# Kernel optimization log

Measured on AMD Instinct MI355X. Metric: run time of the kernel, lower is better.

The kernel has to match this reference:

```python
import jax, jax.numpy as jnp
import numpy as np

OSC_TIME = 10
UNITS = 256
D_IN = 256
BATCH = 32
SEQLEN = 2000


def setup_inputs() -> dict:
    key = jax.random.key(0)
    k1, k2, k3 = jax.random.split(key, 3)
    scale = 1.0 / np.sqrt(UNITS)
    x = jax.random.normal(k1, (BATCH, SEQLEN, D_IN), dtype=jnp.float32)
    W_x = jax.random.normal(k2, (4, 2, D_IN, UNITS), dtype=jnp.float32) * scale
    W_h = jax.random.normal(k3, (4, 2, UNITS, UNITS), dtype=jnp.float32) * scale
    b_x = jnp.zeros((4, 2, UNITS), dtype=jnp.float32)
    b_h = jnp.zeros((4, 2, UNITS), dtype=jnp.float32)
    return {"x": x, "W_x": W_x, "b_x": b_x, "W_h": W_h, "b_h": b_h}


def reference(x, W_x, b_x, W_h, b_h):
    # Subsample every OSC_TIME steps (tf.gather stride)
    xs = x[:, ::OSC_TIME]                       # [B, Ts, D]
    B, Ts, _ = xs.shape
    U = W_h.shape[-1]

    # Precompute input projections for all 4 cells x 2 gates: [4,2,B,Ts,U]
    xp = jnp.einsum('btd,cgdu->cgbtu', xs, W_x) + b_x[:, :, None, None, :]

    h0 = jnp.zeros((4, B, U), dtype=x.dtype)

    def ff_step(h, xp_t):                       # h [4,B,U], xp_t [4,2,B,U]
        hp = jnp.einsum('cbu,cguv->cgbv', h, W_h) + b_h[:, :, None, :]
        g = jax.nn.sigmoid(xp_t + hp)           # [4,2,B,U]
        j, k = g[:, 0], g[:, 1]
        h_new = j * (1.0 - h) + (1.0 - k) * h   # flip-flop update
        return h_new, h_new

    _, hs = jax.lax.scan(ff_step, h0, jnp.moveaxis(xp, 3, 0))  # hs [Ts,4,B,U]
    phi, omega, r, mu = hs[:, 0], hs[:, 1], hs[:, 2], hs[:, 3]  # each [Ts,B,U]

    # Oscillator: emit z = r*cos(phi) then update r, phi; OSC_TIME sub-steps
    def osc_step(carry, _):
        r_t, phi_t = carry
        z = r_t * jnp.cos(phi_t)
        r_n = r_t + (mu - jnp.square(r_t)) * r_t
        phi_n = phi_t + omega
        return (r_n, phi_n), z

    _, zs = jax.lax.scan(osc_step, (r, phi), None, length=OSC_TIME)  # [S,Ts,B,U]
    out = jnp.transpose(zs, (2, 1, 0, 3)).reshape(B, Ts * OSC_TIME, U)
    return out
```

## Files before the change

### kernel.cpp

```cpp
#include <hip/hip_runtime.h>
#include <hip/hip_fp16.h>
#include <stdint.h>

#define TS 200

typedef _Float16 h2_t  __attribute__((ext_vector_type(2)));
typedef _Float16 f16x8 __attribute__((ext_vector_type(8)));
typedef float    f32x4 __attribute__((ext_vector_type(4)));

static __device__ __forceinline__ float fdot2f(uint32_t w, uint32_t h, float acc) {
#if __has_builtin(__builtin_amdgcn_fdot2)
    return __builtin_amdgcn_fdot2(__builtin_bit_cast(h2_t, w),
                                  __builtin_bit_cast(h2_t, h), acc, false);
#else
    h2_t a = __builtin_bit_cast(h2_t, w), b = __builtin_bit_cast(h2_t, h);
    acc = fmaf((float)a.x, (float)b.x, acc);
    acc = fmaf((float)a.y, (float)b.y, acc);
    return acc;
#endif
}

template <int CTRL>
static __device__ __forceinline__ float dpp_add(float x) {
    int m = __builtin_amdgcn_update_dpp(0, __builtin_bit_cast(int, x), CTRL, 0xF, 0xF, true);
    return x + __builtin_bit_cast(float, m);
}

__global__ __launch_bounds__(256) void pack_all(const float* __restrict__ x,
                                                const float* __restrict__ Wx,
                                                const float* __restrict__ Wh,
                                                _Float16* __restrict__ xh,
                                                _Float16* __restrict__ wxt,
                                                uint32_t* __restrict__ wp) {
    int bid = blockIdx.x, tid = threadIdx.x;
    if (bid < 6400) {
        int row = bid, col = tid;
        int b = row / 200, t = row - b * 200;
        xh[(size_t)row * 256 + col] = (_Float16)x[((size_t)(b * 2000 + t * 10)) * 256 + col];
    } else if (bid < 8448) {
        int n = bid - 6400, k = tid;
        wxt[(size_t)n * 256 + k] = (_Float16)Wx[((size_t)((n >> 8) * 256 + k)) * 256 + (n & 255)];
    } else {
        int idx = (bid - 8448) * 256 + tid;
        int e = idx & 3, thr = (idx >> 2) & 511, j = (idx >> 11) & 15;
        int g = (idx >> 15) & 1, c = idx >> 16;
        int vs = thr & 7, uq = (thr >> 3) & 7, wu = thr >> 6;
        int uu = j >> 2, i = j & 3;
        int u = wu * 32 + uq * 4 + uu;
        int v = vs * 32 + i * 8 + e * 2;
        const float* base = Wh + ((size_t)((c * 2 + g) * 256 + v)) * 256 + u;
        h2_t p; p.x = (_Float16)base[0]; p.y = (_Float16)base[256];
        wp[idx] = __builtin_bit_cast(uint32_t, p);
    }
}

__global__ __launch_bounds__(256) void xp_gemm(const _Float16* __restrict__ xh,
                                               const _Float16* __restrict__ wxt,
                                               const float* __restrict__ bxf,
                                               _Float16* __restrict__ xp) {
    __shared__ _Float16 As[128 * 64];
    __shared__ _Float16 Bs[128 * 64];
    const int tid = threadIdx.x;
    const int lane = tid & 63, w = tid >> 6;
    const int m0 = (blockIdx.x >> 4) * 128;
    const int n0 = (blockIdx.x & 15) * 128;
    const int mw = (w & 1) * 64, nw = (w >> 1) * 64;

    f32x4 acc[4][4] = {};

    for (int kb = 0; kb < 4; kb++) {
        const int k0 = kb * 64;
#pragma unroll
        for (int q = 0; q < 4; q++) {
            int ii = w * 4 + q;
            int r = ii * 8 + (lane >> 3);
            int kcol = (lane & 7) * 8;
            const _Float16* ga = xh  + (size_t)(m0 + r) * 256 + k0 + kcol;
            const _Float16* gb = wxt + (size_t)(n0 + r) * 256 + k0 + kcol;
            __builtin_amdgcn_global_load_lds(
                (const __attribute__((address_space(1))) uint32_t*)ga,
                (__attribute__((address_space(3))) uint32_t*)(As + ii * 512), 16, 0, 0);
            __builtin_amdgcn_global_load_lds(
                (const __attribute__((address_space(1))) uint32_t*)gb,
                (__attribute__((address_space(3))) uint32_t*)(Bs + ii * 512), 16, 0, 0);
        }
        __syncthreads();
#pragma unroll
        for (int kc = 0; kc < 2; kc++) {
            f16x8 a[4], b[4];
#pragma unroll
            for (int mt = 0; mt < 4; mt++)
                a[mt] = *(const f16x8*)&As[(mw + mt * 16 + (lane & 15)) * 64 + kc * 32 + (lane >> 4) * 8];
#pragma unroll
            for (int nt = 0; nt < 4; nt++)
                b[nt] = *(const f16x8*)&Bs[(nw + nt * 16 + (lane & 15)) * 64 + kc * 32 + (lane >> 4) * 8];
#pragma unroll
            for (int mt = 0; mt < 4; mt++)
#pragma unroll
                for (int nt = 0; nt < 4; nt++)
                    acc[mt][nt] = __builtin_amdgcn_mfma_f32_16x16x32_f16(a[mt], b[nt], acc[mt][nt], 0, 0, 0);
        }
        __syncthreads();
    }

    const int nl = lane & 15, quad = lane >> 4;
#pragma unroll
    for (int nt = 0; nt < 4; nt++) {
        int n = n0 + nw + nt * 16 + nl;
        float bias = bxf[n];
        int c = n >> 9, gu = n & 511;
#pragma unroll
        for (int mt = 0; mt < 4; mt++)
#pragma unroll
            for (int r = 0; r < 4; r++) {
                int m = m0 + mw + mt * 16 + quad * 4 + r;
                int b = m / 200, t = m - b * 200;
                xp[((size_t)((c * 32 + b) * 200 + t)) * 512 + gu] =
                    (_Float16)(acc[mt][nt][r] + bias);
            }
    }
}

__global__ __launch_bounds__(1024, 4) void recurrence(const _Float16* __restrict__ xp,
                                                      const float* __restrict__ bh,
                                                      const uint32_t* __restrict__ Wp,
                                                      float* __restrict__ hs) {
    const int c = blockIdx.x >> 5;
    const int b = blockIdx.x & 31;
    const int tid = threadIdx.x;
    const int g = tid >> 9;
    const int thr = tid & 511;
    const int lane = tid & 63;
    const int vs = lane & 7;
    const int uq = lane >> 3;
    const int wu = (tid >> 6) & 7;

    __shared__ __align__(16) uint32_t h2s[8 * 20];
    __shared__ float sg[512];

    uint4 w[16];
    {
        const uint4* wb = (const uint4*)Wp + ((size_t)(c * 2 + g) * 16) * 512 + thr;
#pragma unroll
        for (int j = 0; j < 16; j++) w[j] = wb[(size_t)j * 512];
    }
#pragma unroll
    for (int j = 0; j < 16; j++)
        asm volatile("" : "+v"(w[j].x), "+v"(w[j].y), "+v"(w[j].z), "+v"(w[j].w));

    const int u_w = wu * 32 + uq * 4 + vs;
    float bias = 0.f;
    const _Float16* xpb = nullptr;
    if (vs < 4) {
        bias = bh[(c * 2 + g) * 256 + u_w];
        xpb = xp + ((size_t)((c * 32 + b) * 200)) * 512 + g * 256 + u_w;
    }

    float hreg = 0.f;
    if (tid < 160) h2s[tid] = 0u;
    __syncthreads();

    const size_t hsb = (size_t)((c * 32 + b) * 200) * 256 + tid;

    for (int t = 0; t < TS; t++) {
        float xpv = 0.f;
        if (vs < 4) xpv = (float)xpb[(size_t)t * 512];

        uint4 hh[4];
#pragma unroll
        for (int i = 0; i < 4; i++) hh[i] = *(const uint4*)(h2s + vs * 20 + i * 4);

        float acc[4] = {0.f, 0.f, 0.f, 0.f};
#pragma unroll
        for (int uu = 0; uu < 4; uu++)
#pragma unroll
            for (int i = 0; i < 4; i++) {
                acc[uu] = fdot2f(w[uu * 4 + i].x, hh[i].x, acc[uu]);
                acc[uu] = fdot2f(w[uu * 4 + i].y, hh[i].y, acc[uu]);
                acc[uu] = fdot2f(w[uu * 4 + i].z, hh[i].z, acc[uu]);
                acc[uu] = fdot2f(w[uu * 4 + i].w, hh[i].w, acc[uu]);
            }
#pragma unroll
        for (int uu = 0; uu < 4; uu++) {
            float a = acc[uu];
            a = dpp_add<0xB1>(a);
            a = dpp_add<0x4E>(a);
            a = dpp_add<0x141>(a);
            acc[uu] = a;
        }
        if (vs < 4) {
            float s = (vs == 0 ? acc[0] : vs == 1 ? acc[1] : vs == 2 ? acc[2] : acc[3])
                      + xpv + bias;
            sg[u_w * 2 + g] = 1.f / (1.f + __expf(-s));
        }
        __syncthreads();
        if (tid < 256) {
            float2 jk = *(const float2*)(sg + tid * 2);
            float hn = jk.x + hreg * (1.f - jk.x - jk.y);
            hreg = hn;
            hs[hsb + (size_t)t * 256] = hn;
            ((_Float16*)h2s)[(tid >> 5) * 40 + (tid & 31)] = (_Float16)hn;
        }
        __syncthreads();
    }
}

__global__ __launch_bounds__(256) void osc(const float* __restrict__ hs,
                                           float* __restrict__ out) {
    int tid = blockIdx.x * 256 + threadIdx.x;
    const int cstride = 32 * 200 * 256;
    int u = tid & 255;
    int bt = tid >> 8;
    int t = bt % 200, b = bt / 200;
    float phi   = hs[0 * cstride + tid];
    float omega = hs[1 * cstride + tid];
    float r     = hs[2 * cstride + tid];
    float mu    = hs[3 * cstride + tid];
    float* o = out + ((size_t)(b * 2000 + t * 10)) * 256 + u;
#pragma unroll
    for (int s = 0; s < 10; s++) {
        o[(size_t)s * 256] = r * __cosf(phi);
        r = r + (mu - r * r) * r;
        phi = phi + omega;
    }
}

extern "C" void kernel_launch(void* const* d_in, const int* in_sizes, int n_in,
                              void* d_out, int out_size, void* d_ws, size_t ws_size,
                              hipStream_t stream) {
    const float* x  = (const float*)d_in[0];
    const float* Wx = (const float*)d_in[1];
    const float* bx = (const float*)d_in[2];
    const float* Wh = (const float*)d_in[3];
    const float* bh = (const float*)d_in[4];
    float* out = (float*)d_out;

    char* ws = (char*)d_ws;
    const size_t XP = (size_t)4 * 32 * 200 * 512 * 2;
    const size_t HS = (size_t)4 * 32 * 200 * 256 * 4;
    const size_t XH = (size_t)6400 * 256 * 2;

    _Float16* xp  = (_Float16*)ws;
    float*    hs  = (float*)(ws + XP);
    _Float16* xh  = (_Float16*)(ws + XP);
    _Float16* wxt = (_Float16*)(ws + XP + XH);
    uint32_t* wp  = (uint32_t*)(ws + XP + HS);

    pack_all<<<9472, 256, 0, stream>>>(x, Wx, Wh, xh, wxt, wp);
    xp_gemm<<<800, 256, 0, stream>>>(xh, wxt, bx, xp);
    recurrence<<<128, 1024, 0, stream>>>(xp, bh, wp, hs);
    osc<<<6400, 256, 0, stream>>>(hs, out);
}
```

Baseline: 390.1 us.

## Fuse both gates per wave and double-buffer hidden state to halve barriers

The recurrence work mapping changes so that each wave computes both j and k gates for a pair of units. The flip-flop update is then done in registers via DPP lane moves instead of through shared memory. The hidden-state buffer is double-buffered, which removes one of the two __syncthreads per timestep and the sg shared array. The Wh packing layout is changed to match. The cost is more cross-lane DPP shuffles, and the sigmoid is now computed in every lane rather than only in lanes with vs<4.

```diff
diff --git a/kernel.cpp b/kernel.cpp
--- a/kernel.cpp
+++ b/kernel.cpp
@@ -24,6 +24,11 @@
 static __device__ __forceinline__ float dpp_add(float x) {
     int m = __builtin_amdgcn_update_dpp(0, __builtin_bit_cast(int, x), CTRL, 0xF, 0xF, true);
     return x + __builtin_bit_cast(float, m);
+}
+template <int CTRL>
+static __device__ __forceinline__ float dpp_mov(float x) {
+    int m = __builtin_amdgcn_update_dpp(0, __builtin_bit_cast(int, x), CTRL, 0xF, 0xF, true);
+    return __builtin_bit_cast(float, m);
 }
 
 __global__ __launch_bounds__(256) void pack_all(const float* __restrict__ x,
@@ -42,11 +47,14 @@
         wxt[(size_t)n * 256 + k] = (_Float16)Wx[((size_t)((n >> 8) * 256 + k)) * 256 + (n & 255)];
     } else {
         int idx = (bid - 8448) * 256 + tid;
-        int e = idx & 3, thr = (idx >> 2) & 511, j = (idx >> 11) & 15;
-        int g = (idx >> 15) & 1, c = idx >> 16;
-        int vs = thr & 7, uq = (thr >> 3) & 7, wu = thr >> 6;
-        int uu = j >> 2, i = j & 3;
-        int u = wu * 32 + uq * 4 + uu;
+        int e   = idx & 3;
+        int thr = (idx >> 2) & 1023;
+        int j   = (idx >> 12) & 15;
+        int c   = idx >> 16;
+        int a = j >> 2, i = j & 3;
+        int uu = a >> 1, g = a & 1;
+        int vs = thr & 7, uq = (thr >> 3) & 7, wv = thr >> 6;
+        int u = (wv * 8 + uq) * 2 + uu;
         int v = vs * 32 + i * 8 + e * 2;
         const float* base = Wh + ((size_t)((c * 2 + g) * 256 + v)) * 256 + u;
         h2_t p; p.x = (_Float16)base[0]; p.y = (_Float16)base[256];
@@ -121,85 +129,90 @@
     }
 }
 
-__global__ __launch_bounds__(1024, 4) void recurrence(const _Float16* __restrict__ xp,
-                                                      const float* __restrict__ bh,
-                                                      const uint32_t* __restrict__ Wp,
-                                                      float* __restrict__ hs) {
-    const int c = blockIdx.x >> 5;
-    const int b = blockIdx.x & 31;
+__global__ __attribute__((amdgpu_flat_work_group_size(1024, 1024),
+                          amdgpu_waves_per_eu(4, 4)))
+void recurrence(const _Float16* __restrict__ xp,
+                const float* __restrict__ bh,
+                const uint32_t* __restrict__ Wp,
+                float* __restrict__ hs) {
+    const int cb  = blockIdx.x;
+    const int c   = cb >> 5;
     const int tid = threadIdx.x;
-    const int g = tid >> 9;
-    const int thr = tid & 511;
     const int lane = tid & 63;
     const int vs = lane & 7;
     const int uq = lane >> 3;
-    const int wu = (tid >> 6) & 7;
-
-    __shared__ __align__(16) uint32_t h2s[8 * 20];
-    __shared__ float sg[512];
+    const int wv = tid >> 6;
+    const int upair = wv * 8 + uq;
+    const int u0 = upair * 2;
+
+    __shared__ __align__(16) uint32_t h2s[2][160];
 
     uint4 w[16];
     {
-        const uint4* wb = (const uint4*)Wp + ((size_t)(c * 2 + g) * 16) * 512 + thr;
-#pragma unroll
-        for (int j = 0; j < 16; j++) w[j] = wb[(size_t)j * 512];
+        const uint4* wb = (const uint4*)Wp + (size_t)c * 16 * 1024 + tid;
+#pragma unroll
+        for (int j = 0; j < 16; j++) w[j] = wb[(size_t)j * 1024];
     }
 #pragma unroll
     for (int j = 0; j < 16; j++)
         asm volatile("" : "+v"(w[j].x), "+v"(w[j].y), "+v"(w[j].z), "+v"(w[j].w));
 
-    const int u_w = wu * 32 + uq * 4 + vs;
     float bias = 0.f;
     const _Float16* xpb = nullptr;
     if (vs < 4) {
-        bias = bh[(c * 2 + g) * 256 + u_w];
-        xpb = xp + ((size_t)((c * 32 + b) * 200)) * 512 + g * 256 + u_w;
+        int g_sel = vs & 1, u_sel = u0 + (vs >> 1);
+        bias = bh[(c * 2 + g_sel) * 256 + u_sel];
+        xpb  = xp + (size_t)cb * 200 * 512 + g_sel * 256 + u_sel;
     }
 
     float hreg = 0.f;
-    if (tid < 160) h2s[tid] = 0u;
+    if (tid < 160) { h2s[0][tid] = 0u; }
     __syncthreads();
 
-    const size_t hsb = (size_t)((c * 32 + b) * 200) * 256 + tid;
+    float* hsb = hs + (size_t)cb * 200 * 256 + u0;
+
+    const uint32_t* wf = (const uint32_t*)w;
 
     for (int t = 0; t < TS; t++) {
+        const uint32_t* hbuf = h2s[t & 1];
+        uint32_t* hnext = h2s[(t + 1) & 1];
+
         float xpv = 0.f;
         if (vs < 4) xpv = (float)xpb[(size_t)t * 512];
 
         uint4 hh[4];
 #pragma unroll
-        for (int i = 0; i < 4; i++) hh[i] = *(const uint4*)(h2s + vs * 20 + i * 4);
+        for (int i = 0; i < 4; i++) hh[i] = *(const uint4*)(hbuf + vs * 20 + i * 4);
+        const uint32_t* hf = (const uint32_t*)hh;
 
         float acc[4] = {0.f, 0.f, 0.f, 0.f};
 #pragma unroll
-        for (int uu = 0; uu < 4; uu++)
-#pragma unroll
-            for (int i = 0; i < 4; i++) {
-                acc[uu] = fdot2f(w[uu * 4 + i].x, hh[i].x, acc[uu]);
-                acc[uu] = fdot2f(w[uu * 4 + i].y, hh[i].y, acc[uu]);
-                acc[uu] = fdot2f(w[uu * 4 + i].z, hh[i].z, acc[uu]);
-                acc[uu] = fdot2f(w[uu * 4 + i].w, hh[i].w, acc[uu]);
-            }
-#pragma unroll
-        for (int uu = 0; uu < 4; uu++) {
-            float a = acc[uu];
-            a = dpp_add<0xB1>(a);
-            a = dpp_add<0x4E>(a);
-            a = dpp_add<0x141>(a);
-            acc[uu] = a;
-        }
-        if (vs < 4) {
-            float s = (vs == 0 ? acc[0] : vs == 1 ? acc[1] : vs == 2 ? acc[2] : acc[3])
-                      + xpv + bias;
-            sg[u_w * 2 + g] = 1.f / (1.f + __expf(-s));
-        }
-        __syncthreads();
-        if (tid < 256) {
-            float2 jk = *(const float2*)(sg + tid * 2);
-            float hn = jk.x + hreg * (1.f - jk.x - jk.y);
-            hreg = hn;
-            hs[hsb + (size_t)t * 256] = hn;
-            ((_Float16*)h2s)[(tid >> 5) * 40 + (tid & 31)] = (_Float16)hn;
+        for (int i = 0; i < 4; i++)
+#pragma unroll
+            for (int cmp = 0; cmp < 4; cmp++)
+#pragma unroll
+                for (int a = 0; a < 4; a++)
+                    acc[a] = fdot2f(wf[(a * 4 + i) * 4 + cmp], hf[i * 4 + cmp], acc[a]);
+
+#pragma unroll
+        for (int a = 0; a < 4; a++) {
+            float v = acc[a];
+            v = dpp_add<0xB1>(v);
+            v = dpp_add<0x4E>(v);
+            v = dpp_add<0x141>(v);
+            acc[a] = v;
+        }
+        float s = (vs == 0) ? acc[0] : (vs == 1) ? acc[1] : (vs == 2) ? acc[2] : acc[3];
+        s += xpv + bias;
+        float sig = 1.f / (1.f + __expf(-s));
+        float kg = dpp_mov<0xB1>(sig);
+        float hn = sig + hreg * (1.f - sig - kg);
+        hreg = hn;
+        float hn1 = dpp_mov<0x4E>(hn);
+        if (vs == 0) {
+            h2_t p; p.x = (_Float16)hn; p.y = (_Float16)hn1;
+            hnext[(upair >> 4) * 20 + (upair & 15)] = __builtin_bit_cast(uint32_t, p);
+            *(float2*)(hsb + (size_t)t * 256) = make_float2(hn, hn1);
         }
         __syncthreads();
     }
```

Result: faster. 374.2 us (-4.1%).
